# Optimization experiments

Hardware: AMD Instinct MI355X
Metric: run time of the kernel (lower is better)

## Reference

```python
import math
import jax, jax.numpy as jnp
import numpy as np

B, L, H = 8, 2048, 256


def setup_inputs() -> dict:
    key = jax.random.key(0)
    k1, k2, k3, k4, k5 = jax.random.split(key, 5)
    inputs = jax.random.normal(k1, (B, L, H), dtype=jnp.float32)
    scale = 1.0 / math.sqrt(H)
    Wq = jax.random.normal(k2, (H, H), dtype=jnp.float32) * scale
    Wk = jax.random.normal(k3, (H, H), dtype=jnp.float32) * scale
    Wv = jax.random.normal(k4, (H, H), dtype=jnp.float32) * scale
    lens = jax.random.randint(k5, (B,), L // 2, L + 1)
    lens = lens.at[0].set(L)  # original assumes max(lens) == L
    return {"inputs": inputs, "Wq": Wq, "Wk": Wk, "Wv": Wv, "lens": lens}


def reference(inputs, Wq, Wk, Wv, lens):
    # nn.Linear(bias=False): y = x @ W.T
    Q = jnp.einsum('blh,oh->blo', inputs, Wq)
    K = jnp.einsum('blh,oh->blo', inputs, Wk)
    V = jnp.einsum('blh,oh->blo', inputs, Wv)
    d = Q.shape[-1]
    alpha = jnp.einsum('bqd,bkd->bqk', Q, K) / math.sqrt(d)  # [B, L, L]
    # key-padding mask: [B, 1, L] broadcast over query dim (matches expand)
    mask = (jnp.arange(L)[None, :] < lens[:, None])[:, None, :]
    NEG = jnp.float32(-2.0 ** 31)
    alpha = jnp.where(mask, alpha, NEG)
    alpha = jax.nn.softmax(alpha, axis=2)
    out = jnp.einsum('bqk,bkd->bqd', alpha, V)
    return out
```

## Files before the change

### kernel.cpp

```cpp
#include <hip/hip_runtime.h>

#define BB 8
#define LL 2048
#define DD 256

typedef _Float16 half8 __attribute__((ext_vector_type(8)));
typedef float floatx4 __attribute__((ext_vector_type(4)));
typedef unsigned short ushort8 __attribute__((ext_vector_type(8)));

__device__ inline unsigned short f2h(float f) {
  _Float16 h = (_Float16)f;
  return __builtin_bit_cast(unsigned short, h);
}

#define GLD16(src, ldsbase)                                                    \
  __builtin_amdgcn_global_load_lds(                                           \
      (const __attribute__((address_space(1))) unsigned int*)(src),           \
      (__attribute__((address_space(3))) unsigned int*)(ldsbase), 16, 0, 0)

__global__ __launch_bounds__(256) void wcvt(
    const float* __restrict__ Wq, const float* __restrict__ Wk,
    const float* __restrict__ Wv, unsigned short* __restrict__ Wh) {
  const int bm = blockIdx.x >> 5;
  const float* src = (bm == 0) ? Wq : (bm == 1) ? Wk : Wv;
  const int off = (blockIdx.x & 31) * 2048 + threadIdx.x * 8;
  float4 a = *(const float4*)(src + off);
  float4 b = *(const float4*)(src + off + 4);
  ushort8 u = {f2h(a.x), f2h(a.y), f2h(a.z), f2h(a.w),
               f2h(b.x), f2h(b.y), f2h(b.z), f2h(b.w)};
  *(ushort8*)(Wh + bm * 65536 + off) = u;
}

__global__ __launch_bounds__(256) void proj(
    const float* __restrict__ x, const unsigned short* __restrict__ Wh,
    unsigned short* __restrict__ Qb, unsigned short* __restrict__ Kb,
    unsigned short* __restrict__ VT) {
  __shared__ __attribute__((aligned(16))) unsigned char smem[53248];
  unsigned short* Ws = (unsigned short*)smem;
  unsigned short* tile = (unsigned short*)(smem + 32768);
  const int t = threadIdx.x;
  const int wave = t >> 6, lane = t & 63, quad = lane >> 4, m16 = lane & 15;
  const int l0g = blockIdx.x * 32;
  const int b = l0g >> 11, lb = l0g & 2047;

  half8 xf[2][8];
#pragma unroll
  for (int mt = 0; mt < 2; ++mt) {
    const float* xp = x + (size_t)(l0g + mt * 16 + m16) * DD + quad * 8;
#pragma unroll
    for (int kb = 0; kb < 8; ++kb) {
      float4 a = *(const float4*)(xp + kb * 32);
      float4 c = *(const float4*)(xp + kb * 32 + 4);
      ushort8 u = {f2h(a.x), f2h(a.y), f2h(a.z), f2h(a.w),
                   f2h(c.x), f2h(c.y), f2h(c.z), f2h(c.w)};
      xf[mt][kb] = __builtin_bit_cast(half8, u);
    }
  }

  for (int gg = 0; gg < 12; ++gg) {
    const int mat = gg >> 2, og = gg & 3;
#pragma unroll
    for (int c = 0; c < 8; ++c) {
      int ch = c * 256 + t;
      int row = ch >> 5, cc = ch & 31;
      const unsigned short* src = Wh + mat * 65536 +
          (size_t)(og * 64 + row) * DD + ((cc ^ (row & 7)) << 3);
      GLD16(src, smem + (c * 256 + wave * 64) * 16);
    }
    __syncthreads();

    const int ot = og * 4 + wave;
    const int wrow = wave * 16 + m16;
    floatx4 acc[2] = {{0, 0, 0, 0}, {0, 0, 0, 0}};
    if (mat < 2) {
#pragma unroll
      for (int kb = 0; kb < 8; ++kb) {
        half8 wf = __builtin_bit_cast(
            half8, *(const ushort8*)&Ws[wrow * 256 +
                                        (((kb * 4 + quad) ^ (wrow & 7)) << 3)]);
        acc[0] = __builtin_amdgcn_mfma_f32_16x16x32_f16(xf[0][kb], wf,
                                                        acc[0], 0, 0, 0);
        acc[1] = __builtin_amdgcn_mfma_f32_16x16x32_f16(xf[1][kb], wf,
                                                        acc[1], 0, 0, 0);
      }
#pragma unroll
      for (int mt = 0; mt < 2; ++mt)
#pragma unroll
        for (int r = 0; r < 4; ++r)
          tile[(mt * 16 + quad * 4 + r) * 264 + ot * 16 + m16] =
              f2h(acc[mt][r]);
    } else {
#pragma unroll
      for (int kb = 0; kb < 8; ++kb) {
        half8 wf = __builtin_bit_cast(
            half8, *(const ushort8*)&Ws[wrow * 256 +
                                        (((kb * 4 + quad) ^ (wrow & 7)) << 3)]);
        acc[0] = __builtin_amdgcn_mfma_f32_16x16x32_f16(wf, xf[0][kb],
                                                        acc[0], 0, 0, 0);
        acc[1] = __builtin_amdgcn_mfma_f32_16x16x32_f16(wf, xf[1][kb],
                                                        acc[1], 0, 0, 0);
      }
#pragma unroll
      for (int mt = 0; mt < 2; ++mt)
#pragma unroll
        for (int r = 0; r < 4; ++r)
          tile[(ot * 16 + quad * 4 + r) * 40 + mt * 16 + m16] =
              f2h(acc[mt][r]);
    }
    __syncthreads();

    if (og == 3) {
      if (mat < 2) {
        unsigned short* Out = mat ? Kb : Qb;
        const int row = t >> 3, c0 = (t & 7) * 8;
#pragma unroll
        for (int i = 0; i < 4; ++i) {
          ushort8 v = *(const ushort8*)&tile[row * 264 + c0 + i * 64];
          *(ushort8*)(Out + (size_t)(l0g + row) * DD + c0 + i * 64) = v;
        }
      } else {
        const int dd = t >> 2, lc = (t & 3) * 8;
#pragma unroll
        for (int p = 0; p < 4; ++p) {
          const int d = p * 64 + dd;
          ushort8 v = *(const ushort8*)&tile[d * 40 + lc];
          *(ushort8*)(VT + ((size_t)(b * DD + d)) * LL + lb + lc) = v;
        }
      }
      __syncthreads();
    }
  }
}

__global__ __launch_bounds__(512, 1) void attn(
    const unsigned short* __restrict__ Qb, const unsigned short* __restrict__ Kb,
    const unsigned short* __restrict__ VT, const int* __restrict__ lens,
    float* __restrict__ out) {
  __shared__ __attribute__((aligned(16))) unsigned char smem[149504];
  const int t = threadIdx.x;
  const int wave = t >> 6, lane = t & 63, quad = lane >> 4, m16 = lane & 15;
  const int grp = wave >> 2, qw = wave & 3, tgl = t & 255;
  unsigned short* Ks = (unsigned short*)(smem + grp * 32768);
  unsigned short* Vs = (unsigned short*)(smem + 65536 + grp * 32768);
  unsigned short* Pw = (unsigned short*)(smem + 131072 + wave * 2304);

  const int b = blockIdx.x;
  const int q0 = blockIdx.y * 64;
  const int len = lens[b];
  const size_t baseQK = (size_t)b * LL * DD;
  const size_t baseVT = (size_t)b * DD * LL;

  half8 qf[8];
  {
    const unsigned short* qrow =
        Qb + baseQK + (size_t)(q0 + qw * 16 + m16) * DD + quad * 8;
    for (int kb = 0; kb < 8; ++kb)
      qf[kb] = __builtin_bit_cast(half8, *(const ushort8*)(qrow + kb * 32));
  }

  floatx4 O[16];
  for (int i = 0; i < 16; ++i) O[i] = (floatx4){0, 0, 0, 0};
  float mrow[4] = {-1e30f, -1e30f, -1e30f, -1e30f};
  float lrow[4] = {0.f, 0.f, 0.f, 0.f};

  ushort8 kreg[8], vreg[8];
  const unsigned short* kbase = Kb + baseQK;
  const unsigned short* vbase = VT + baseVT;

#define LOAD_TILES(KV0)                                                      \
  {                                                                          \
    const unsigned short* kp = kbase + (size_t)(KV0)*DD;                     \
    for (int c = 0; c < 8; ++c)                                              \
      kreg[c] = *(const ushort8*)(kp + (tgl + c * 256) * 8);                 \
    for (int c = 0; c < 8; ++c) {                                            \
      int ch = tgl + c * 256;                                                \
      vreg[c] = *(const ushort8*)(vbase + (size_t)(ch >> 3) * LL + (KV0) +   \
                                  (ch & 7) * 8);                             \
    }                                                                        \
  }

  const int T = (len + 127) >> 7;
  LOAD_TILES(grp * 64);
  asm volatile("" ::: "memory");

  for (int it = 0; it < T; ++it) {
    const int kv0 = it * 128 + grp * 64;
    __syncthreads();
    for (int c = 0; c < 8; ++c) {
      int ch = tgl + c * 256, row = ch >> 5, cc = ch & 31;
      *(ushort8*)&Ks[row * 256 + (cc ^ (row & 7)) * 8] = kreg[c];
    }
    for (int c = 0; c < 8; ++c) {
      int ch = tgl + c * 256, d = ch >> 3, cc = ch & 7;
      *(ushort8*)&Vs[d * 64 + (cc ^ (d & 7)) * 8] = vreg[c];
    }
    __syncthreads();
    if (it + 1 < T) {
      LOAD_TILES(kv0 + 128);
      asm volatile("" ::: "memory");
    }

    if (kv0 < len) {
      floatx4 s[4];
      for (int n = 0; n < 4; ++n) s[n] = (floatx4){0, 0, 0, 0};
      __builtin_amdgcn_s_setprio(1);
      for (int kb = 0; kb < 8; ++kb)
        for (int n = 0; n < 4; ++n) {
          half8 kf = __builtin_bit_cast(
              half8, *(const ushort8*)&Ks[(n * 16 + m16) * 256 +
                                          (((kb * 4 + quad) ^ (m16 & 7)) * 8)]);
          s[n] = __builtin_amdgcn_mfma_f32_16x16x32_f16(qf[kb], kf, s[n], 0, 0, 0);
        }
      __builtin_amdgcn_s_setprio(0);
      float sv[4][4];
      for (int n = 0; n < 4; ++n) {
        bool valid = (kv0 + n * 16 + m16) < len;
        for (int r = 0; r < 4; ++r)
          sv[n][r] = valid ? s[n][r] * 0.0625f : -1e30f;
      }
      float al[4];
      for (int r = 0; r < 4; ++r) {
        float v = fmaxf(fmaxf(sv[0][r], sv[1][r]), fmaxf(sv[2][r], sv[3][r]));
        v = fmaxf(v, __shfl_xor(v, 1));
        v = fmaxf(v, __shfl_xor(v, 2));
        v = fmaxf(v, __shfl_xor(v, 4));
        v = fmaxf(v, __shfl_xor(v, 8));
        float mn = fmaxf(mrow[r], v);
        al[r] = __expf(mrow[r] - mn);
        mrow[r] = mn;
        float sum = 0.f;
        for (int n = 0; n < 4; ++n) {
          float p = __expf(sv[n][r] - mn);
          Pw[(quad * 4 + r) * 72 + n * 16 + m16] = f2h(p);
          sum += p;
        }
        sum += __shfl_xor(sum, 1);
        sum += __shfl_xor(sum, 2);
        sum += __shfl_xor(sum, 4);
        sum += __shfl_xor(sum, 8);
        lrow[r] = lrow[r] * al[r] + sum;
      }
      for (int i = 0; i < 16; ++i)
        for (int r = 0; r < 4; ++r) O[i][r] *= al[r];
      half8 pf0 = __builtin_bit_cast(half8,
                                     *(const ushort8*)&Pw[m16 * 72 + quad * 8]);
      half8 pf1 = __builtin_bit_cast(
          half8, *(const ushort8*)&Pw[m16 * 72 + 32 + quad * 8]);
      __builtin_amdgcn_s_setprio(1);
      for (int nb = 0; nb < 16; ++nb) {
        half8 vf0 = __builtin_bit_cast(
            half8, *(const ushort8*)&Vs[(nb * 16 + m16) * 64 +
                                        ((quad ^ (m16 & 7)) * 8)]);
        O[nb] = __builtin_amdgcn_mfma_f32_16x16x32_f16(pf0, vf0, O[nb], 0, 0, 0);
        half8 vf1 = __builtin_bit_cast(
            half8, *(const ushort8*)&Vs[(nb * 16 + m16) * 64 +
                                        (((4 + quad) ^ (m16 & 7)) * 8)]);
        O[nb] = __builtin_amdgcn_mfma_f32_16x16x32_f16(pf1, vf1, O[nb], 0, 0, 0);
      }
      __builtin_amdgcn_s_setprio(0);
    }
  }
#undef LOAD_TILES

  __syncthreads();
  float* Om = (float*)(smem) + qw * 4112;
  float* ml = (float*)(smem + 65792) + qw * 32;
  if (grp == 1) {
    for (int nb = 0; nb < 16; ++nb)
      for (int r = 0; r < 4; ++r)
        Om[(quad * 4 + r) * 257 + nb * 16 + m16] = O[nb][r];
    if (m16 == 0)
      for (int r = 0; r < 4; ++r) {
        ml[(quad * 4 + r) * 2] = mrow[r];
        ml[(quad * 4 + r) * 2 + 1] = lrow[r];
      }
  }
  __syncthreads();
  if (grp == 0) {
    float a[4], bf[4], inv[4];
    for (int r = 0; r < 4; ++r) {
      float mB = ml[(quad * 4 + r) * 2];
      float lB = ml[(quad * 4 + r) * 2 + 1];
      float m = fmaxf(mrow[r], mB);
      a[r] = __expf(mrow[r] - m);
      bf[r] = __expf(mB - m);
      inv[r] = 1.f / (lrow[r] * a[r] + lB * bf[r]);
    }
    for (int nb = 0; nb < 16; ++nb)
      for (int r = 0; r < 4; ++r) {
        float ob = Om[(quad * 4 + r) * 257 + nb * 16 + m16];
        out[baseQK + (size_t)(q0 + qw * 16 + quad * 4 + r) * DD + nb * 16 +
            m16] = (O[nb][r] * a[r] + ob * bf[r]) * inv[r];
      }
  }
}

extern "C" void kernel_launch(void* const* d_in, const int* in_sizes, int n_in,
                              void* d_out, int out_size, void* d_ws, size_t ws_size,
                              hipStream_t stream) {
  const float* x = (const float*)d_in[0];
  const float* Wq = (const float*)d_in[1];
  const float* Wk = (const float*)d_in[2];
  const float* Wv = (const float*)d_in[3];
  const int* lens = (const int*)d_in[4];
  unsigned short* Qb = (unsigned short*)d_ws;
  unsigned short* Kb = Qb + (size_t)BB * LL * DD;
  unsigned short* VT = Kb + (size_t)BB * LL * DD;
  unsigned short* Wh = VT + (size_t)BB * LL * DD;
  float* out = (float*)d_out;

  wcvt<<<96, 256, 0, stream>>>(Wq, Wk, Wv, Wh);
  proj<<<512, 256, 0, stream>>>(x, Wh, Qb, Kb, VT);
  attn<<<dim3(8, 32), 512, 0, stream>>>(Qb, Kb, VT, lens, out);
}
```

Measured before the change: 166.4 us.

## Fuse weight conversion into projection kernel with register prefetch and larger blocks

Removes the separate fp32-to-fp16 weight conversion kernel; the projection kernel now loads fp32 weights directly, converts them in registers and writes them swizzled into shared memory, prefetching the next weight chunk while computing the current one. Blocks grow to 512 threads covering 64 rows each, halving the number of blocks that reread the weights and dropping one barrier per iteration. This saves a kernel launch and workspace round trip but adds register pressure and uses more LDS per block.

```diff
diff --git a/kernel.cpp b/kernel.cpp
--- a/kernel.cpp
+++ b/kernel.cpp
@@ -13,103 +13,106 @@
   return __builtin_bit_cast(unsigned short, h);
 }
 
-#define GLD16(src, ldsbase)                                                    \
-  __builtin_amdgcn_global_load_lds(                                           \
-      (const __attribute__((address_space(1))) unsigned int*)(src),           \
-      (__attribute__((address_space(3))) unsigned int*)(ldsbase), 16, 0, 0)
-
-__global__ __launch_bounds__(256) void wcvt(
-    const float* __restrict__ Wq, const float* __restrict__ Wk,
-    const float* __restrict__ Wv, unsigned short* __restrict__ Wh) {
-  const int bm = blockIdx.x >> 5;
-  const float* src = (bm == 0) ? Wq : (bm == 1) ? Wk : Wv;
-  const int off = (blockIdx.x & 31) * 2048 + threadIdx.x * 8;
-  float4 a = *(const float4*)(src + off);
-  float4 b = *(const float4*)(src + off + 4);
-  ushort8 u = {f2h(a.x), f2h(a.y), f2h(a.z), f2h(a.w),
-               f2h(b.x), f2h(b.y), f2h(b.z), f2h(b.w)};
-  *(ushort8*)(Wh + bm * 65536 + off) = u;
-}
-
-__global__ __launch_bounds__(256) void proj(
-    const float* __restrict__ x, const unsigned short* __restrict__ Wh,
+__global__ __launch_bounds__(512) void proj(
+    const float* __restrict__ x, const float* __restrict__ Wq,
+    const float* __restrict__ Wk, const float* __restrict__ Wv,
     unsigned short* __restrict__ Qb, unsigned short* __restrict__ Kb,
     unsigned short* __restrict__ VT) {
-  __shared__ __attribute__((aligned(16))) unsigned char smem[53248];
+  __shared__ __attribute__((aligned(16))) unsigned char smem[69632];
   unsigned short* Ws = (unsigned short*)smem;
   unsigned short* tile = (unsigned short*)(smem + 32768);
   const int t = threadIdx.x;
   const int wave = t >> 6, lane = t & 63, quad = lane >> 4, m16 = lane & 15;
-  const int l0g = blockIdx.x * 32;
+  const int ot = wave >> 1, p = wave & 1;
+  const int l0g = blockIdx.x * 64;
   const int b = l0g >> 11, lb = l0g & 2047;
 
   half8 xf[2][8];
 #pragma unroll
-  for (int mt = 0; mt < 2; ++mt) {
-    const float* xp = x + (size_t)(l0g + mt * 16 + m16) * DD + quad * 8;
+  for (int j = 0; j < 2; ++j) {
+    const float* xp =
+        x + (size_t)(l0g + (p * 2 + j) * 16 + m16) * DD + quad * 8;
 #pragma unroll
     for (int kb = 0; kb < 8; ++kb) {
       float4 a = *(const float4*)(xp + kb * 32);
       float4 c = *(const float4*)(xp + kb * 32 + 4);
       ushort8 u = {f2h(a.x), f2h(a.y), f2h(a.z), f2h(a.w),
                    f2h(c.x), f2h(c.y), f2h(c.z), f2h(c.w)};
-      xf[mt][kb] = __builtin_bit_cast(half8, u);
-    }
-  }
-
-  for (int gg = 0; gg < 12; ++gg) {
-    const int mat = gg >> 2, og = gg & 3;
-#pragma unroll
-    for (int c = 0; c < 8; ++c) {
-      int ch = c * 256 + t;
-      int row = ch >> 5, cc = ch & 31;
-      const unsigned short* src = Wh + mat * 65536 +
-          (size_t)(og * 64 + row) * DD + ((cc ^ (row & 7)) << 3);
-      GLD16(src, smem + (c * 256 + wave * 64) * 16);
-    }
+      xf[j][kb] = __builtin_bit_cast(half8, u);
+    }
+  }
+
+  float4 wA[4], wB[4];
+#define LOADW(G)                                                              \
+  {                                                                           \
+    const int mat_ = (G) >> 2, og_ = (G)&3;                                   \
+    const float* Wm = (mat_ == 0) ? Wq : (mat_ == 1) ? Wk : Wv;               \
+    _Pragma("unroll") for (int c = 0; c < 4; ++c) {                           \
+      int ch = c * 512 + t, row = ch >> 5, cc = ch & 31;                      \
+      const float* s = Wm + (size_t)(og_ * 64 + row) * DD + cc * 8;           \
+      wA[c] = *(const float4*)s;                                              \
+      wB[c] = *(const float4*)(s + 4);                                        \
+    }                                                                         \
+  }
+
+  LOADW(0);
+  asm volatile("" ::: "memory");
+
+  for (int g = 0; g < 12; ++g) {
+    const int mat = g >> 2, og = g & 3;
     __syncthreads();
-
-    const int ot = og * 4 + wave;
-    const int wrow = wave * 16 + m16;
+#pragma unroll
+    for (int c = 0; c < 4; ++c) {
+      int ch = c * 512 + t, row = ch >> 5, cc = ch & 31;
+      ushort8 u = {f2h(wA[c].x), f2h(wA[c].y), f2h(wA[c].z), f2h(wA[c].w),
+                   f2h(wB[c].x), f2h(wB[c].y), f2h(wB[c].z), f2h(wB[c].w)};
+      *(ushort8*)&Ws[row * 256 + ((cc ^ (row & 7)) << 3)] = u;
+    }
+    __syncthreads();
+    if (g < 11) {
+      LOADW(g + 1);
+      asm volatile("" ::: "memory");
+    }
+
     floatx4 acc[2] = {{0, 0, 0, 0}, {0, 0, 0, 0}};
     if (mat < 2) {
 #pragma unroll
       for (int kb = 0; kb < 8; ++kb) {
         half8 wf = __builtin_bit_cast(
-            half8, *(const ushort8*)&Ws[wrow * 256 +
-                                        (((kb * 4 + quad) ^ (wrow & 7)) << 3)]);
+            half8, *(const ushort8*)&Ws[(ot * 16 + m16) * 256 +
+                                        (((kb * 4 + quad) ^ (m16 & 7)) << 3)]);
         acc[0] = __builtin_amdgcn_mfma_f32_16x16x32_f16(xf[0][kb], wf,
                                                         acc[0], 0, 0, 0);
         acc[1] = __builtin_amdgcn_mfma_f32_16x16x32_f16(xf[1][kb], wf,
                                                         acc[1], 0, 0, 0);
       }
 #pragma unroll
-      for (int mt = 0; mt < 2; ++mt)
+      for (int j = 0; j < 2; ++j)
 #pragma unroll
         for (int r = 0; r < 4; ++r)
-          tile[(mt * 16 + quad * 4 + r) * 264 + ot * 16 + m16] =
-              f2h(acc[mt][r]);
+          tile[((p * 2 + j) * 16 + quad * 4 + r) * 264 + og * 64 + ot * 16 +
+               m16] = f2h(acc[j][r]);
     } else {
 #pragma unroll
       for (int kb = 0; kb < 8; ++kb) {
         half8 wf = __builtin_bit_cast(
-            half8, *(const ushort8*)&Ws[wrow * 256 +
-                                        (((kb * 4 + quad) ^ (wrow & 7)) << 3)]);
+            half8, *(const ushort8*)&Ws[(ot * 16 + m16) * 256 +
+                                        (((kb * 4 + quad) ^ (m16 & 7)) << 3)]);
         acc[0] = __builtin_amdgcn_mfma_f32_16x16x32_f16(wf, xf[0][kb],
                                                         acc[0], 0, 0, 0);
         acc[1] = __builtin_amdgcn_mfma_f32_16x16x32_f16(wf, xf[1][kb],
                                                         acc[1], 0, 0, 0);
       }
 #pragma unroll
-      for (int mt = 0; mt < 2; ++mt)
+      for (int j = 0; j < 2; ++j)
 #pragma unroll
         for (int r = 0; r < 4; ++r)
-          tile[(ot * 16 + quad * 4 + r) * 40 + mt * 16 + m16] =
-              f2h(acc[mt][r]);
-    }
-    __syncthreads();
+          tile[(og * 64 + ot * 16 + quad * 4 + r) * 72 + (p * 2 + j) * 16 +
+               m16] = f2h(acc[j][r]);
+    }
 
     if (og == 3) {
+      __syncthreads();
       if (mat < 2) {
         unsigned short* Out = mat ? Kb : Qb;
         const int row = t >> 3, c0 = (t & 7) * 8;
@@ -119,17 +122,16 @@
           *(ushort8*)(Out + (size_t)(l0g + row) * DD + c0 + i * 64) = v;
         }
       } else {
-        const int dd = t >> 2, lc = (t & 3) * 8;
-#pragma unroll
-        for (int p = 0; p < 4; ++p) {
-          const int d = p * 64 + dd;
-          ushort8 v = *(const ushort8*)&tile[d * 40 + lc];
+#pragma unroll
+        for (int c = 0; c < 4; ++c) {
+          int ch = c * 512 + t, d = ch >> 3, lc = (ch & 7) * 8;
+          ushort8 v = *(const ushort8*)&tile[d * 72 + lc];
           *(ushort8*)(VT + ((size_t)(b * DD + d)) * LL + lb + lc) = v;
         }
       }
-      __syncthreads();
-    }
-  }
+    }
+  }
+#undef LOADW
 }
 
 __global__ __launch_bounds__(512, 1) void attn(
@@ -306,10 +308,8 @@
   unsigned short* Qb = (unsigned short*)d_ws;
   unsigned short* Kb = Qb + (size_t)BB * LL * DD;
   unsigned short* VT = Kb + (size_t)BB * LL * DD;
-  unsigned short* Wh = VT + (size_t)BB * LL * DD;
   float* out = (float*)d_out;
 
-  wcvt<<<96, 256, 0, stream>>>(Wq, Wk, Wv, Wh);
-  proj<<<512, 256, 0, stream>>>(x, Wh, Qb, Kb, VT);
+  proj<<<256, 512, 0, stream>>>(x, Wq, Wk, Wv, Qb, Kb, VT);
   attn<<<dim3(8, 32), 512, 0, stream>>>(Qb, Kb, VT, lens, out);
 }
```

After: 168.9 us. About the same (+1.5%).
